# Kernel optimization log

Measured on AMD Instinct MI355X. Metric: run time of the kernel, lower is better.

Reference implementation:

```python
import jax, jax.numpy as jnp
import numpy as np

N_SAMPLE = 32
BETA = 1.0


def setup_inputs() -> dict:
    key = jax.random.key(0)
    k1, k2 = jax.random.split(key)
    # small scales so the gaussian kernel over 512 dims does not underflow
    x = jax.random.normal(k1, (2048, 512), dtype=jnp.float32) * 0.05
    W = jax.random.normal(k2, (512, 2048), dtype=jnp.float32) * 0.02  # Dense kernel [in, hidden]
    return {"x": x, "W": W}


def reference(x, W):
    B, H = x.shape[0], W.shape[1]
    # Encoder: h = x W ; z = softmax(h * beita)
    h = x @ W                                   # [B, H]
    z = jax.nn.softmax(h * BETA, axis=-1)       # [B, H]
    # Sampler: tf.random.categorical treats z (probs) as LOGITS -> same here.
    key = jax.random.key(42)
    # tf gives [B, n_sample]; jax categorical with shape=(NS, B) then .T matches that,
    # and the original code then RESHAPES (not transposes) to [NS, B] -> replicate scramble.
    samp = jax.random.categorical(key, z, axis=-1, shape=(N_SAMPLE, B)).T  # [B, NS]
    samp = samp.reshape(N_SAMPLE, B)            # faithful reshape, not transpose
    onehot = jax.nn.one_hot(samp, H, dtype=x.dtype)          # [NS, B, H]
    # tensordot(onehot, W, axes=[2,1]) -> gather rows of W^T as dense matmul
    x_decoded = jnp.einsum('nbh,dh->nbd', onehot, W)          # [NS, B, D]
    # gauss(x[None], x_decoded), var=1
    diff = x[None, :, :] - x_decoded                          # [NS, B, D]
    coeff = 1.0 / jnp.sqrt(2.0 * jnp.pi)
    temp = coeff * jnp.exp(-0.5 * jnp.sum(diff * diff, axis=-1))  # [NS, B]
    weight = temp / jnp.mean(temp, axis=0)                    # broadcast over NS
    return (h, z, onehot, x_decoded, weight)
```

## Files before the change

### kernel.cpp

```cpp
#include <hip/hip_runtime.h>
#include <stdint.h>
#include <math.h>

static constexpr int BDIM = 2048;
static constexpr int HDIM = 2048;
static constexpr int DDIM = 512;
static constexpr int NSAMP = 32;

static constexpr size_t OFF_H  = 0;
static constexpr size_t OFF_Z  = (size_t)BDIM * HDIM;
static constexpr size_t OFF_OH = OFF_Z + (size_t)BDIM * HDIM;
static constexpr size_t OFF_XD = OFF_OH + (size_t)NSAMP * BDIM * HDIM;
static constexpr size_t OFF_W  = OFF_XD + (size_t)NSAMP * BDIM * DDIM;

static constexpr size_t WS_WT    = 0;
static constexpr size_t WS_XB    = 1048576;
static constexpr size_t WS_WTB   = WS_XB + 524288;
static constexpr size_t WS_SAMP  = WS_WTB + 524288;
static constexpr size_t WS_TEMP  = WS_SAMP + 65536;
static constexpr size_t WS_DELTA = WS_TEMP + 65536;

typedef __attribute__((ext_vector_type(8))) short short8;
typedef __attribute__((ext_vector_type(4))) float f32x4;

__device__ __forceinline__ ushort f2bf(float f) {
  uint32_t x = __float_as_uint(f);
  return (ushort)((x + 0x7FFFu + ((x >> 16) & 1u)) >> 16);
}

__global__ __launch_bounds__(256) void cast_x_kernel(const float* __restrict__ x,
                                                     ushort* __restrict__ xb) {
  const int i = (blockIdx.x * 256 + threadIdx.x) * 4;
  float4 v = *(const float4*)(x + i);
  ushort4 o = {f2bf(v.x), f2bf(v.y), f2bf(v.z), f2bf(v.w)};
  *(ushort4*)(xb + i) = o;
}

__global__ __launch_bounds__(256) void transpose_kernel(const float* __restrict__ W,
                                                        float* __restrict__ Wt,
                                                        ushort* __restrict__ Wtb) {
  __shared__ float tile[32][33];
  const int tx = threadIdx.x & 31, ty = threadIdx.x >> 5;
  const int bx = blockIdx.x;
  const int by = blockIdx.y;
#pragma unroll
  for (int i = 0; i < 32; i += 8)
    tile[ty + i][tx] = W[(size_t)(by * 32 + ty + i) * HDIM + bx * 32 + tx];
  __syncthreads();
#pragma unroll
  for (int i = 0; i < 32; i += 8) {
    float v = tile[tx][ty + i];
    const size_t o = (size_t)(bx * 32 + ty + i) * DDIM + by * 32 + tx;
    Wt[o] = v;
    Wtb[o] = f2bf(v);
  }
}

__global__ __launch_bounds__(256) void gemm_mfma_kernel(const ushort* __restrict__ xb,
                                                        const ushort* __restrict__ wtb,
                                                        float* __restrict__ h) {
  __shared__ short As[128][72];
  __shared__ short Bs[128][72];
  const int tid = threadIdx.x;
  const int bm = blockIdx.y * 128, bn = blockIdx.x * 128;
  const int wave = tid >> 6, lane = tid & 63;
  const int wm = (wave >> 1) * 64, wn = (wave & 1) * 64;
  const int lrow = lane & 15, lk = (lane >> 4) * 8;

  f32x4 acc[4][4] = {};

  const int srow = tid >> 3;
  const int scol = (tid & 7) * 8;

  for (int k0 = 0; k0 < DDIM; k0 += 64) {
#pragma unroll
    for (int p = 0; p < 4; ++p) {
      const int r = srow + p * 32;
      short8 av = *(const short8*)(xb + (size_t)(bm + r) * DDIM + k0 + scol);
      short8 bv = *(const short8*)(wtb + (size_t)(bn + r) * DDIM + k0 + scol);
      *(short8*)&As[r][scol] = av;
      *(short8*)&Bs[r][scol] = bv;
    }
    __syncthreads();
#pragma unroll
    for (int kk = 0; kk < 64; kk += 32) {
      short8 af[4], bf[4];
#pragma unroll
      for (int i = 0; i < 4; ++i) {
        af[i] = *(const short8*)&As[wm + i * 16 + lrow][kk + lk];
        bf[i] = *(const short8*)&Bs[wn + i * 16 + lrow][kk + lk];
      }
#pragma unroll
      for (int i = 0; i < 4; ++i)
#pragma unroll
        for (int j = 0; j < 4; ++j)
          acc[i][j] = __builtin_amdgcn_mfma_f32_16x16x32_bf16(af[i], bf[j], acc[i][j], 0, 0, 0);
    }
    __syncthreads();
  }
#pragma unroll
  for (int i = 0; i < 4; ++i)
#pragma unroll
    for (int j = 0; j < 4; ++j)
#pragma unroll
      for (int rg = 0; rg < 4; ++rg) {
        const int row = bm + wm + i * 16 + (lane >> 4) * 4 + rg;
        const int col = bn + wn + j * 16 + (lane & 15);
        h[(size_t)row * HDIM + col] = acc[i][j][rg];
      }
}

__global__ __launch_bounds__(256) void softmax_kernel(const float* __restrict__ h,
                                                      float* __restrict__ z,
                                                      float* __restrict__ rowDelta) {
  const int b = blockIdx.x;
  const int tid = threadIdx.x;
  const float* row = h + (size_t)b * HDIM;
  float* zrow = z + (size_t)b * HDIM;
  __shared__ float red[256], red2[256];

  float vals[8];
  float vmax = -INFINITY, vmin = INFINITY;
#pragma unroll
  for (int k = 0; k < 8; ++k) {
    float v = row[tid + (k << 8)];
    vals[k] = v;
    vmax = fmaxf(vmax, v);
    vmin = fminf(vmin, v);
  }
  red[tid] = vmax; red2[tid] = vmin;
  __syncthreads();
  for (int s = 128; s > 0; s >>= 1) {
    if (tid < s) {
      red[tid] = fmaxf(red[tid], red[tid + s]);
      red2[tid] = fminf(red2[tid], red2[tid + s]);
    }
    __syncthreads();
  }
  const float rmax = red[0], rmin = red2[0];
  __syncthreads();

  float e[8];
  float lsum = 0.f;
#pragma unroll
  for (int k = 0; k < 8; ++k) {
    e[k] = expf(vals[k] - rmax);
    lsum += e[k];
  }
  red[tid] = lsum;
  __syncthreads();
  for (int s = 128; s > 0; s >>= 1) {
    if (tid < s) red[tid] += red[tid + s];
    __syncthreads();
  }
  const float rsum = red[0];
#pragma unroll
  for (int k = 0; k < 8; ++k) zrow[tid + (k << 8)] = e[k] / rsum;
  if (tid == 0) rowDelta[b] = (1.0f - expf(rmin - rmax)) / rsum;
}

__device__ __forceinline__ void threefry_0_42(uint32_t x0, uint32_t x1,
                                              uint32_t& o0, uint32_t& o1) {
  const uint32_t ks0 = 0u, ks1 = 42u, ks2 = 0x1BD11BDAu ^ 0u ^ 42u;
  x0 += ks0; x1 += ks1;
#define TF_R(r) { x0 += x1; x1 = (x1 << (r)) | (x1 >> (32 - (r))); x1 ^= x0; }
  TF_R(13) TF_R(15) TF_R(26) TF_R(6)   x0 += ks1; x1 += ks2 + 1u;
  TF_R(17) TF_R(29) TF_R(16) TF_R(24)  x0 += ks2; x1 += ks0 + 2u;
  TF_R(13) TF_R(15) TF_R(26) TF_R(6)   x0 += ks0; x1 += ks1 + 3u;
  TF_R(17) TF_R(29) TF_R(16) TF_R(24)  x0 += ks1; x1 += ks2 + 4u;
  TF_R(13) TF_R(15) TF_R(26) TF_R(6)   x0 += ks2; x1 += ks0 + 5u;
#undef TF_R
  o0 = x0; o1 = x1;
}

__device__ __forceinline__ float bits_to_u(uint32_t bits) {
  float f = __uint_as_float((bits >> 9) | 0x3f800000u) - 1.0f;
  return (f == 0.0f) ? 1.1754943508222875e-38f : f;
}

__global__ __launch_bounds__(256) void sample_kernel(const float* __restrict__ z,
                                                     const float* __restrict__ rowDelta,
                                                     int* __restrict__ samp) {
  const int r = blockIdx.x;
  const int b = r & (BDIM - 1);
  const int tid = threadIdx.x;
  const int lane = tid & 63;
  const int wav = tid >> 6;
  const float* zrow = z + (size_t)b * HDIM;

  __shared__ uint32_t wmax[4];
  __shared__ double wbest[4];
  __shared__ int wbh[4];

  const uint32_t base = (uint32_t)r << 11;
  uint32_t bb[8];
  uint32_t m23 = 0u;
#pragma unroll
  for (int k = 0; k < 8; ++k) {
    uint32_t o0, o1;
    threefry_0_42(0u, base + (uint32_t)(tid + (k << 8)), o0, o1);
    bb[k] = (o0 ^ o1) >> 9;
    m23 = max(m23, bb[k]);
  }
#pragma unroll
  for (int off = 32; off > 0; off >>= 1)
    m23 = max(m23, (uint32_t)__shfl_xor((int)m23, off, 64));
  if (lane == 0) wmax[wav] = m23;
  __syncthreads();
  m23 = max(max(wmax[0], wmax[1]), max(wmax[2], wmax[3]));
  const float umax = bits_to_u(m23 << 9);

  const float dpad = rowDelta[b] + 3e-4f;
  float uthr = expf(-expf(-(-logf(-logf(umax)) - dpad)));
  uthr = __uint_as_float(__float_as_uint(uthr) - 4u);
  uint32_t thr23 = __float_as_uint(1.0f + uthr) & 0x7FFFFFu;
  if (thr23 > 0u) thr23 -= 1u;

  double best = -1e300; int bh = 0x7fffffff;
#pragma unroll
  for (int k = 0; k < 8; ++k) {
    if (bb[k] >= thr23 || bb[k] == m23) {
      const int hh = tid + (k << 8);
      const float uk = bits_to_u(bb[k] << 9);
      double s = -log(-log((double)uk)) + (double)zrow[hh];
      if (s > best || (s == best && hh < bh)) { best = s; bh = hh; }
    }
  }
#pragma unroll
  for (int off = 32; off > 0; off >>= 1) {
    double so = __shfl_down(best, off, 64);
    int ho = __shfl_down(bh, off, 64);
    if (so > best || (so == best && ho < bh)) { best = so; bh = ho; }
  }
  if (lane == 0) { wbest[wav] = best; wbh[wav] = bh; }
  __syncthreads();
  if (tid == 0) {
#pragma unroll
    for (int w2 = 1; w2 < 4; ++w2) {
      if (wbest[w2] > best || (wbest[w2] == best && wbh[w2] < bh)) {
        best = wbest[w2]; bh = wbh[w2];
      }
    }
    samp[r] = bh;
  }
}

__device__ __forceinline__ int scrambled_samp(const int* samp, int j) {
  return samp[((j & 31) << 11) | (j >> 5)];
}

__global__ __launch_bounds__(256) void onehot_kernel(const int* __restrict__ samp,
                                                     float* __restrict__ oh) {
  const size_t idx4 = (size_t)blockIdx.x * 256 + threadIdx.x;
  const size_t el = idx4 << 2;
  const int j = (int)(el >> 11);
  const int h0 = (int)(el & 2047);
  const int s = scrambled_samp(samp, j);
  const unsigned d = (unsigned)(s - h0);
  float4 v;
  v.x = (d == 0u) ? 1.f : 0.f;
  v.y = (d == 1u) ? 1.f : 0.f;
  v.z = (d == 2u) ? 1.f : 0.f;
  v.w = (d == 3u) ? 1.f : 0.f;
  ((float4*)oh)[idx4] = v;
}

__global__ __launch_bounds__(256) void xdec_kernel(const float* __restrict__ x,
                                                   const float* __restrict__ Wt,
                                                   const int* __restrict__ samp,
                                                   float* __restrict__ xd,
                                                   float* __restrict__ temp) {
  const int j = blockIdx.x * 2 + (threadIdx.x >> 7);
  const int t = threadIdx.x & 127;
  const int s = scrambled_samp(samp, j);
  const int c = j & (BDIM - 1);

  const float4 wv = ((const float4*)(Wt + (size_t)s * DDIM))[t];
  const float4 xv = ((const float4*)(x + (size_t)c * DDIM))[t];
  ((float4*)(xd + (size_t)j * DDIM))[t] = wv;

  const float dx = xv.x - wv.x, dy = xv.y - wv.y, dz = xv.z - wv.z, dw = xv.w - wv.w;
  float ss = dx * dx + dy * dy + dz * dz + dw * dw;

  __shared__ float sred[256];
  sred[threadIdx.x] = ss;
  __syncthreads();
  for (int st = 64; st > 0; st >>= 1) {
    if (t < st) sred[threadIdx.x] += sred[threadIdx.x + st];
    __syncthreads();
  }
  if (t == 0) temp[j] = 0.3989422804014327f * expf(-0.5f * sred[threadIdx.x]);
}

__global__ __launch_bounds__(256) void weight_kernel(const float* __restrict__ temp,
                                                     float* __restrict__ wout) {
  const int c = blockIdx.x * 256 + threadIdx.x;
  if (c >= BDIM) return;
  float sum = 0.f;
#pragma unroll
  for (int a = 0; a < NSAMP; ++a) sum += temp[a * BDIM + c];
  const float mean = sum / 32.0f;
#pragma unroll
  for (int a = 0; a < NSAMP; ++a) wout[a * BDIM + c] = temp[a * BDIM + c] / mean;
}

extern "C" void kernel_launch(void* const* d_in, const int* in_sizes, int n_in,
                              void* d_out, int out_size, void* d_ws, size_t ws_size,
                              hipStream_t stream) {
  (void)in_sizes; (void)n_in; (void)out_size; (void)ws_size;
  const float* x = (const float*)d_in[0];
  const float* W = (const float*)d_in[1];
  float* out = (float*)d_out;

  float* h  = out + OFF_H;
  float* z  = out + OFF_Z;
  float* oh = out + OFF_OH;
  float* xd = out + OFF_XD;
  float* wo = out + OFF_W;

  float* ws = (float*)d_ws;
  float* Wt = ws + WS_WT;
  ushort* xb = (ushort*)(ws + WS_XB);
  ushort* Wtb = (ushort*)(ws + WS_WTB);
  int* samp = (int*)(ws + WS_SAMP);
  float* temp = ws + WS_TEMP;
  float* rowDelta = ws + WS_DELTA;

  cast_x_kernel<<<1024, 256, 0, stream>>>(x, xb);
  transpose_kernel<<<dim3(64, 16), 256, 0, stream>>>(W, Wt, Wtb);
  gemm_mfma_kernel<<<dim3(16, 16), 256, 0, stream>>>(xb, Wtb, h);
  softmax_kernel<<<2048, 256, 0, stream>>>(h, z, rowDelta);
  sample_kernel<<<65536, 256, 0, stream>>>(z, rowDelta, samp);
  onehot_kernel<<<131072, 256, 0, stream>>>(samp, oh);
  xdec_kernel<<<32768, 256, 0, stream>>>(x, Wt, samp, xd, temp);
  weight_kernel<<<8, 256, 0, stream>>>(temp, wo);
}
```

Measured before the change: 1.005 ms.

## Build one-hot via memset plus scatter, wave-per-row sampling, shuffle softmax reductions

The one-hot output is now produced by a bulk hipMemsetAsync zero fill followed by a small scatter kernel that writes only the single 1.0 per row. This replaces a kernel that computed and stored every element. The sampling kernel now assigns one row to each wavefront instead of one row to each 256-thread block, so block-level syncs and shared-memory merges go away. The softmax reductions switch from tree reductions in shared memory to wave shuffles. The memset still has to write the full 512MB, so the gain depends on the fill engine running faster than the old kernel, and each thread in the sampler now holds more registers.

After: 979.3 us. 1.03x faster.

```diff
diff --git a/kernel.cpp b/kernel.cpp
--- a/kernel.cpp
+++ b/kernel.cpp
@@ -115,9 +115,10 @@
                                                       float* __restrict__ rowDelta) {
   const int b = blockIdx.x;
   const int tid = threadIdx.x;
+  const int lane = tid & 63, wav = tid >> 6;
   const float* row = h + (size_t)b * HDIM;
   float* zrow = z + (size_t)b * HDIM;
-  __shared__ float red[256], red2[256];
+  __shared__ float wmaxs[4], wmins[4], wsums[4];
 
   float vals[8];
   float vmax = -INFINITY, vmin = INFINITY;
@@ -128,17 +129,15 @@
     vmax = fmaxf(vmax, v);
     vmin = fminf(vmin, v);
   }
-  red[tid] = vmax; red2[tid] = vmin;
+#pragma unroll
+  for (int off = 32; off > 0; off >>= 1) {
+    vmax = fmaxf(vmax, __shfl_xor(vmax, off, 64));
+    vmin = fminf(vmin, __shfl_xor(vmin, off, 64));
+  }
+  if (lane == 0) { wmaxs[wav] = vmax; wmins[wav] = vmin; }
   __syncthreads();
-  for (int s = 128; s > 0; s >>= 1) {
-    if (tid < s) {
-      red[tid] = fmaxf(red[tid], red[tid + s]);
-      red2[tid] = fminf(red2[tid], red2[tid + s]);
-    }
-    __syncthreads();
-  }
-  const float rmax = red[0], rmin = red2[0];
-  __syncthreads();
+  const float rmax = fmaxf(fmaxf(wmaxs[0], wmaxs[1]), fmaxf(wmaxs[2], wmaxs[3]));
+  const float rmin = fminf(fminf(wmins[0], wmins[1]), fminf(wmins[2], wmins[3]));
 
   float e[8];
   float lsum = 0.f;
@@ -147,13 +146,11 @@
     e[k] = expf(vals[k] - rmax);
     lsum += e[k];
   }
-  red[tid] = lsum;
+#pragma unroll
+  for (int off = 32; off > 0; off >>= 1) lsum += __shfl_xor(lsum, off, 64);
+  if (lane == 0) wsums[wav] = lsum;
   __syncthreads();
-  for (int s = 128; s > 0; s >>= 1) {
-    if (tid < s) red[tid] += red[tid + s];
-    __syncthreads();
-  }
-  const float rsum = red[0];
+  const float rsum = wsums[0] + wsums[1] + wsums[2] + wsums[3];
 #pragma unroll
   for (int k = 0; k < 8; ++k) zrow[tid + (k << 8)] = e[k] / rsum;
   if (tid == 0) rowDelta[b] = (1.0f - expf(rmin - rmax)) / rsum;
@@ -181,33 +178,25 @@
 __global__ __launch_bounds__(256) void sample_kernel(const float* __restrict__ z,
                                                      const float* __restrict__ rowDelta,
                                                      int* __restrict__ samp) {
-  const int r = blockIdx.x;
+  const int wav = threadIdx.x >> 6;
+  const int lane = threadIdx.x & 63;
+  const int r = blockIdx.x * 4 + wav;
   const int b = r & (BDIM - 1);
-  const int tid = threadIdx.x;
-  const int lane = tid & 63;
-  const int wav = tid >> 6;
   const float* zrow = z + (size_t)b * HDIM;
 
-  __shared__ uint32_t wmax[4];
-  __shared__ double wbest[4];
-  __shared__ int wbh[4];
-
   const uint32_t base = (uint32_t)r << 11;
-  uint32_t bb[8];
+  uint32_t bb[32];
   uint32_t m23 = 0u;
 #pragma unroll
-  for (int k = 0; k < 8; ++k) {
+  for (int k = 0; k < 32; ++k) {
     uint32_t o0, o1;
-    threefry_0_42(0u, base + (uint32_t)(tid + (k << 8)), o0, o1);
+    threefry_0_42(0u, base + (uint32_t)(lane + (k << 6)), o0, o1);
     bb[k] = (o0 ^ o1) >> 9;
     m23 = max(m23, bb[k]);
   }
 #pragma unroll
   for (int off = 32; off > 0; off >>= 1)
     m23 = max(m23, (uint32_t)__shfl_xor((int)m23, off, 64));
-  if (lane == 0) wmax[wav] = m23;
-  __syncthreads();
-  m23 = max(max(wmax[0], wmax[1]), max(wmax[2], wmax[3]));
   const float umax = bits_to_u(m23 << 9);
 
   const float dpad = rowDelta[b] + 3e-4f;
@@ -218,9 +207,9 @@
 
   double best = -1e300; int bh = 0x7fffffff;
 #pragma unroll
-  for (int k = 0; k < 8; ++k) {
+  for (int k = 0; k < 32; ++k) {
     if (bb[k] >= thr23 || bb[k] == m23) {
-      const int hh = tid + (k << 8);
+      const int hh = lane + (k << 6);
       const float uk = bits_to_u(bb[k] << 9);
       double s = -log(-log((double)uk)) + (double)zrow[hh];
       if (s > best || (s == best && hh < bh)) { best = s; bh = hh; }
@@ -232,37 +221,18 @@
     int ho = __shfl_down(bh, off, 64);
     if (so > best || (so == best && ho < bh)) { best = so; bh = ho; }
   }
-  if (lane == 0) { wbest[wav] = best; wbh[wav] = bh; }
-  __syncthreads();
-  if (tid == 0) {
-#pragma unroll
-    for (int w2 = 1; w2 < 4; ++w2) {
-      if (wbest[w2] > best || (wbest[w2] == best && wbh[w2] < bh)) {
-        best = wbest[w2]; bh = wbh[w2];
-      }
-    }
-    samp[r] = bh;
-  }
+  if (lane == 0) samp[r] = bh;
 }
 
 __device__ __forceinline__ int scrambled_samp(const int* samp, int j) {
   return samp[((j & 31) << 11) | (j >> 5)];
 }
 
-__global__ __launch_bounds__(256) void onehot_kernel(const int* __restrict__ samp,
-                                                     float* __restrict__ oh) {
-  const size_t idx4 = (size_t)blockIdx.x * 256 + threadIdx.x;
-  const size_t el = idx4 << 2;
-  const int j = (int)(el >> 11);
-  const int h0 = (int)(el & 2047);
+__global__ __launch_bounds__(256) void onehot_scatter_kernel(const int* __restrict__ samp,
+                                                             float* __restrict__ oh) {
+  const int j = blockIdx.x * 256 + threadIdx.x;
   const int s = scrambled_samp(samp, j);
-  const unsigned d = (unsigned)(s - h0);
-  float4 v;
-  v.x = (d == 0u) ? 1.f : 0.f;
-  v.y = (d == 1u) ? 1.f : 0.f;
-  v.z = (d == 2u) ? 1.f : 0.f;
-  v.w = (d == 3u) ? 1.f : 0.f;
-  ((float4*)oh)[idx4] = v;
+  oh[(size_t)j * HDIM + s] = 1.0f;
 }
 
 __global__ __launch_bounds__(256) void xdec_kernel(const float* __restrict__ x,
@@ -326,12 +296,14 @@
   float* temp = ws + WS_TEMP;
   float* rowDelta = ws + WS_DELTA;
 
+  hipMemsetAsync(oh, 0, (size_t)NSAMP * BDIM * HDIM * sizeof(float), stream);
+
   cast_x_kernel<<<1024, 256, 0, stream>>>(x, xb);
   transpose_kernel<<<dim3(64, 16), 256, 0, stream>>>(W, Wt, Wtb);
   gemm_mfma_kernel<<<dim3(16, 16), 256, 0, stream>>>(xb, Wtb, h);
   softmax_kernel<<<2048, 256, 0, stream>>>(h, z, rowDelta);
-  sample_kernel<<<65536, 256, 0, stream>>>(z, rowDelta, samp);
-  onehot_kernel<<<131072, 256, 0, stream>>>(samp, oh);
+  sample_kernel<<<16384, 256, 0, stream>>>(z, rowDelta, samp);
+  onehot_scatter_kernel<<<256, 256, 0, stream>>>(samp, oh);
   xdec_kernel<<<32768, 256, 0, stream>>>(x, Wt, samp, xd, temp);
   weight_kernel<<<8, 256, 0, stream>>>(temp, wo);
 }
```
